# Optimization experiments

Hardware: AMD Instinct MI355X
Metric: run time of the kernel (lower is better)

The kernel has to match this reference:

```python
import jax, jax.numpy as jnp
import numpy as np

N_NODES = 50000
N_EDGES = 800000
N_GRAPHS = 64
IN_C = 256      # num_commodities
HID = 256       # hidden_units
HID2 = HID // 2
N_DCS = 64


def setup_inputs() -> dict:
    key = jax.random.key(0)
    ks = jax.random.split(key, 8)
    x = jax.random.normal(ks[0], (N_NODES, IN_C), dtype=jnp.float32)
    edge_index = jax.random.randint(ks[1], (2, N_EDGES), 0, N_NODES, dtype=jnp.int32)
    # sorted graph-membership ids; even partition guarantees no empty graph
    batch = ((jnp.arange(N_NODES) * N_GRAPHS) // N_NODES).astype(jnp.int32)
    s1 = 1.0 / np.sqrt(IN_C)
    s2 = 1.0 / np.sqrt(HID)
    s3 = 1.0 / np.sqrt(HID2)
    W1 = jax.random.normal(ks[2], (IN_C, HID), dtype=jnp.float32) * s1
    b1 = jnp.zeros((HID,), dtype=jnp.float32)
    W2 = jax.random.normal(ks[3], (HID, HID2), dtype=jnp.float32) * s2
    b2 = jnp.zeros((HID2,), dtype=jnp.float32)
    Wm = jax.random.normal(ks[4], (HID2, N_DCS), dtype=jnp.float32) * s3
    bm = jax.random.normal(ks[5], (N_DCS,), dtype=jnp.float32) * s3
    return {"x": x, "edge_index": edge_index, "batch": batch,
            "W1": W1, "b1": b1, "W2": W2, "b2": b2, "Wm": Wm, "bm": bm}


def gcn_conv(x, W, b, src, dst, n_nodes):
    """PyG GCNConv: D^{-1/2}(A+I)D^{-1/2} X W + b (self-loops added)."""
    h = x @ W                                    # [N, out]
    ones = jnp.ones(src.shape[0], dtype=h.dtype)
    deg = jax.ops.segment_sum(ones, dst, num_segments=n_nodes) + 1.0  # +1 self-loop
    dis = jax.lax.rsqrt(deg)                     # deg >= 1, safe
    norm = dis[src] * dis[dst]                   # [E]
    agg = jax.ops.segment_sum(h[src] * norm[:, None], dst, num_segments=n_nodes)
    agg = agg + h * (dis * dis)[:, None]         # self-loop contribution
    return agg + b


def reference(x, edge_index, batch, W1, b1, W2, b2, Wm, bm):
    src, dst = edge_index[0], edge_index[1]
    n = x.shape[0]
    bx = jax.nn.relu(gcn_conv(x, W1, b1, src, dst, n))
    cx = jax.nn.relu(gcn_conv(bx, W2, b2, src, dst, n))
    px = jax.ops.segment_max(cx, batch, num_segments=N_GRAPHS)  # global max pool
    return px @ Wm + bm                           # [N_GRAPHS, N_DCS]
```

## Files before the change

kernel.cpp:

```cpp
#include <hip/hip_runtime.h>
#include <cstdint>


typedef _Float16 half4v __attribute__((ext_vector_type(4)));
typedef _Float16 half8v __attribute__((ext_vector_type(8)));
typedef float f32x4 __attribute__((ext_vector_type(4)));

__device__ __forceinline__ void gl_lds16(const void* g, void* l) {
  __builtin_amdgcn_global_load_lds(
      (const __attribute__((address_space(1))) unsigned int*)g,
      (__attribute__((address_space(3))) unsigned int*)l, 16, 0, 0);
}

__global__ void count_deg_k(const int* __restrict__ dst, int* __restrict__ deg, int E) {
  int e = blockIdx.x * blockDim.x + threadIdx.x;
  if (e < E) atomicAdd(&deg[dst[e]], 1);
}

__global__ void dis_k(const int* __restrict__ deg, float* __restrict__ dis, int n) {
  int i = blockIdx.x * blockDim.x + threadIdx.x;
  if (i < n) dis[i] = 1.0f / sqrtf((float)deg[i] + 1.0f);
}

__global__ void scan1_k(const int* __restrict__ deg, int* __restrict__ blksum, int n) {
  __shared__ int sd[256];
  int i = blockIdx.x * 256 + threadIdx.x;
  sd[threadIdx.x] = (i < n) ? deg[i] : 0;
  __syncthreads();
  for (int s = 128; s > 0; s >>= 1) {
    if (threadIdx.x < s) sd[threadIdx.x] += sd[threadIdx.x + s];
    __syncthreads();
  }
  if (threadIdx.x == 0) blksum[blockIdx.x] = sd[0];
}

__global__ void scan2_k(const int* __restrict__ blksum, int* __restrict__ blkoff, int nb) {
  __shared__ int sd[256];
  int v = (threadIdx.x < nb) ? blksum[threadIdx.x] : 0;
  sd[threadIdx.x] = v;
  __syncthreads();
  for (int d = 1; d < 256; d <<= 1) {
    int t = (threadIdx.x >= d) ? sd[threadIdx.x - d] : 0;
    __syncthreads();
    sd[threadIdx.x] += t;
    __syncthreads();
  }
  if (threadIdx.x < nb) blkoff[threadIdx.x] = sd[threadIdx.x] - v;
}

__global__ void scan3_k(const int* __restrict__ deg, const int* __restrict__ blkoff,
                        int* __restrict__ offs, int n) {
  __shared__ int sd[256];
  int i = blockIdx.x * 256 + threadIdx.x;
  int v = (i < n) ? deg[i] : 0;
  sd[threadIdx.x] = v;
  __syncthreads();
  for (int d = 1; d < 256; d <<= 1) {
    int t = (threadIdx.x >= d) ? sd[threadIdx.x - d] : 0;
    __syncthreads();
    sd[threadIdx.x] += t;
    __syncthreads();
  }
  if (i < n) offs[i] = blkoff[blockIdx.x] + sd[threadIdx.x] - v;
  if (i == n - 1) offs[n] = blkoff[blockIdx.x] + sd[threadIdx.x];
}

__global__ void fill_csr_k(const int* __restrict__ src, const int* __restrict__ dst,
                           const int* __restrict__ offs, int* __restrict__ cursor,
                           int* __restrict__ csr, int E) {
  int e = blockIdx.x * blockDim.x + threadIdx.x;
  if (e >= E) return;
  int d = dst[e];
  int pos = atomicAdd(&cursor[d], 1);
  csr[offs[d] + pos] = src[e];
}

__global__ void cvt_x_k(const float* __restrict__ in, _Float16* __restrict__ out, int n4) {
  int i = blockIdx.x * blockDim.x + threadIdx.x;
  if (i < n4) {
    float4 v = ((const float4*)in)[i];
    half4v o = {(_Float16)v.x, (_Float16)v.y, (_Float16)v.z, (_Float16)v.w};
    ((half4v*)out)[i] = o;
  }
}

__global__ void cvtT_k(const float* __restrict__ W, _Float16* __restrict__ Wt, int K, int N) {
  int idx = blockIdx.x * 256 + threadIdx.x;
  if (idx < K * N) {
    int k = idx / N, c = idx - k * N;
    Wt[(size_t)c * K + k] = (_Float16)W[idx];
  }
}

#define GBM 128
#define GBN 128
#define GBK 32

__global__ __launch_bounds__(256) void gemm_f16(const _Float16* __restrict__ A,
                                                const _Float16* __restrict__ Bt,
                                                _Float16* __restrict__ C,
                                                int M, int N, int K) {
  __shared__ _Float16 As[GBM * GBK];
  __shared__ _Float16 Bs[GBN * GBK];
  const int tid = threadIdx.x;
  const int lane = tid & 63;
  const int wave = tid >> 6;
  const int wm = wave >> 1, wn = wave & 1;
  const int row0 = blockIdx.x * GBM;
  const int col0 = blockIdx.y * GBN;

  f32x4 acc[4][4] = {};

  const int kbase = (lane >> 4) * 8;
  const _Float16* aSrc[2];
  _Float16* aDst[2];
  const _Float16* bSrc[2];
  _Float16* bDst[2];
#pragma unroll
  for (int h = 0; h < 2; ++h) {
    int fl = h * 4 + wave;
    int row = h * 64 + wave * 16 + (lane & 15);
    int gr = row0 + row;
    if (gr > M - 1) gr = M - 1;
    aSrc[h] = A + (size_t)gr * K + kbase;
    aDst[h] = As + fl * 512;
    int gc = col0 + row;
    bSrc[h] = Bt + (size_t)gc * K + kbase;
    bDst[h] = Bs + fl * 512;
  }

  for (int k0 = 0; k0 < K; k0 += GBK) {
    gl_lds16(aSrc[0] + k0, aDst[0]);
    gl_lds16(aSrc[1] + k0, aDst[1]);
    gl_lds16(bSrc[0] + k0, bDst[0]);
    gl_lds16(bSrc[1] + k0, bDst[1]);
    __syncthreads();

    half8v af[4], bf[4];
#pragma unroll
    for (int m = 0; m < 4; ++m)
      af[m] = *(const half8v*)(As + (wm * 4 + m) * 512 + lane * 8);
#pragma unroll
    for (int nj = 0; nj < 4; ++nj)
      bf[nj] = *(const half8v*)(Bs + (wn * 4 + nj) * 512 + lane * 8);
#pragma unroll
    for (int m = 0; m < 4; ++m)
#pragma unroll
      for (int nj = 0; nj < 4; ++nj)
        acc[m][nj] = __builtin_amdgcn_mfma_f32_16x16x32_f16(af[m], bf[nj], acc[m][nj], 0, 0, 0);
    __syncthreads();
  }

#pragma unroll
  for (int m = 0; m < 4; ++m) {
#pragma unroll
    for (int nj = 0; nj < 4; ++nj) {
      int col = col0 + wn * 64 + nj * 16 + (lane & 15);
#pragma unroll
      for (int r = 0; r < 4; ++r) {
        int row = row0 + wm * 64 + m * 16 + (lane >> 4) * 4 + r;
        if (row < M) C[(size_t)row * N + col] = (_Float16)acc[m][nj][r];
      }
    }
  }
}

template <int C, bool POOL>
__global__ __launch_bounds__(256) void agg_k(const _Float16* __restrict__ h,
                                             const float* __restrict__ dis,
                                             const int* __restrict__ offs,
                                             const int* __restrict__ csr,
                                             const float* __restrict__ bias,
                                             const int* __restrict__ batch,
                                             void* __restrict__ outv, int n) {
  constexpr int LPR = C / 8;
  constexpr int EPW = 64 / LPR;
  const int tid = threadIdx.x;
  const int lane = tid & 63;
  const int wave = tid >> 6;
  const int slot = lane / LPR;
  const int ch0 = (lane % LPR) * 8;

  const int wid = blockIdx.x * 4 + wave;
  const bool valid = wid < n;
  const int node = valid ? wid : n - 1;

  const int beg = offs[node], end = offs[node + 1];
  float acc[8] = {};
  for (int jb = beg; jb < end; jb += EPW * 4) {
#pragma unroll
    for (int u = 0; u < 4; ++u) {
      int e = jb + u * EPW + slot;
      int ec = e < end ? e : end - 1;
      int s = csr[ec];
      float w = (e < end) ? dis[s] : 0.f;
      half8v hv = *(const half8v*)(h + (size_t)s * C + ch0);
#pragma unroll
      for (int v = 0; v < 8; ++v) acc[v] = fmaf((float)hv[v], w, acc[v]);
    }
  }

  if constexpr (EPW == 4) {
#pragma unroll
    for (int v = 0; v < 8; ++v) {
      acc[v] += __shfl_xor(acc[v], 16);
      acc[v] += __shfl_xor(acc[v], 32);
    }
  } else {
#pragma unroll
    for (int v = 0; v < 8; ++v) acc[v] += __shfl_xor(acc[v], 32);
  }

  const float di = dis[node];
  half8v sv = *(const half8v*)(h + (size_t)node * C + ch0);
  float4 blo = *(const float4*)(bias + ch0);
  float4 bhi = *(const float4*)(bias + ch0 + 4);
  const float bb[8] = {blo.x, blo.y, blo.z, blo.w, bhi.x, bhi.y, bhi.z, bhi.w};
  float res[8];
#pragma unroll
  for (int v = 0; v < 8; ++v)
    res[v] = fmaxf(acc[v] * di + (float)sv[v] * (di * di) + bb[v], 0.f);

  if constexpr (!POOL) {
    if (valid && lane < LPR) {
      half8v r;
#pragma unroll
      for (int v = 0; v < 8; ++v) r[v] = (_Float16)res[v];
      *(half8v*)((_Float16*)outv + (size_t)node * C + ch0) = r;
    }
  } else {
    __shared__ float pres[4][C];
    __shared__ int pg[4];
    __shared__ int uni;
    const int g = valid ? batch[node] : -1 - wave;
    if (lane < LPR) {
      *(f32x4*)&pres[wave][ch0] = f32x4{res[0], res[1], res[2], res[3]};
      *(f32x4*)&pres[wave][ch0 + 4] = f32x4{res[4], res[5], res[6], res[7]};
    }
    if (lane == 0) pg[wave] = g;
    __syncthreads();
    if (tid == 0) uni = (pg[0] == pg[1] && pg[1] == pg[2] && pg[2] == pg[3] && pg[0] >= 0);
    __syncthreads();
    float* px = (float*)outv;
    if (uni) {
      if (tid < C) {
        float m = fmaxf(fmaxf(pres[0][tid], pres[1][tid]),
                        fmaxf(pres[2][tid], pres[3][tid]));
        atomicMax((int*)&px[(size_t)pg[0] * C + tid], __float_as_int(m));
      }
    } else {
#pragma unroll
      for (int wv = 0; wv < 4; ++wv) {
        int gg = pg[wv];
        if (gg >= 0 && tid < C)
          atomicMax((int*)&px[(size_t)gg * C + tid], __float_as_int(pres[wv][tid]));
      }
    }
  }
}

__global__ void final_mm_k(const float* __restrict__ px, const float* __restrict__ Wm,
                           const float* __restrict__ bm, float* __restrict__ out) {
  int g = blockIdx.x;
  int c = threadIdx.x;
  float acc = bm[c];
#pragma unroll 8
  for (int k = 0; k < 128; ++k)
    acc = fmaf(px[g * 128 + k], Wm[k * 64 + c], acc);
  out[g * 64 + c] = acc;
}

extern "C" void kernel_launch(void* const* d_in, const int* in_sizes, int n_in,
                              void* d_out, int out_size, void* d_ws, size_t ws_size,
                              hipStream_t stream) {
  const float* x     = (const float*)d_in[0];
  const int*   ei    = (const int*)d_in[1];
  const int*   batch = (const int*)d_in[2];
  const float* W1    = (const float*)d_in[3];
  const float* b1    = (const float*)d_in[4];
  const float* W2    = (const float*)d_in[5];
  const float* b2    = (const float*)d_in[6];
  const float* Wm    = (const float*)d_in[7];
  const float* bm    = (const float*)d_in[8];
  float* out = (float*)d_out;

  const int E = in_sizes[1] / 2;
  const int n = in_sizes[2];
  const int IN_C = 256, HID = 256, HID2 = 128, NG = 64;
  const int* src = ei;
  const int* dst = ei + E;

  char* w = (char*)d_ws;
  size_t off = 0;
  auto alloc = [&](size_t bytes) -> void* {
    void* p = w + off;
    off = (off + bytes + 255) & ~(size_t)255;
    return p;
  };
  const int nb = (n + 255) / 256;
  int*      deg    = (int*)alloc((size_t)n * 4);
  int*      cursor = (int*)alloc((size_t)n * 4);
  float*    dis    = (float*)alloc((size_t)n * 4);
  int*      offs   = (int*)alloc((size_t)(n + 1) * 4);
  int*      blksum = (int*)alloc((size_t)nb * 4);
  int*      blkoff = (int*)alloc((size_t)nb * 4);
  int*      csr    = (int*)alloc((size_t)E * 4);
  float*    px     = (float*)alloc((size_t)NG * HID2 * 4);
  _Float16* xh     = (_Float16*)alloc((size_t)n * IN_C * 2);
  _Float16* Wt1    = (_Float16*)alloc((size_t)HID * IN_C * 2);
  _Float16* Wt2    = (_Float16*)alloc((size_t)HID2 * HID * 2);
  _Float16* bufA   = (_Float16*)alloc((size_t)n * HID * 2);
  _Float16* bufB   = (_Float16*)alloc((size_t)n * HID * 2);
  _Float16* h1 = bufA;
  _Float16* bx = bufB;
  _Float16* h2 = bufA;

  hipMemsetAsync(deg, 0, (size_t)n * 4, stream);
  hipMemsetAsync(cursor, 0, (size_t)n * 4, stream);
  hipMemsetAsync(px, 0, (size_t)NG * HID2 * 4, stream);

  count_deg_k<<<(E + 255) / 256, 256, 0, stream>>>(dst, deg, E);
  dis_k<<<(n + 255) / 256, 256, 0, stream>>>(deg, dis, n);
  scan1_k<<<nb, 256, 0, stream>>>(deg, blksum, n);
  scan2_k<<<1, 256, 0, stream>>>(blksum, blkoff, nb);
  scan3_k<<<nb, 256, 0, stream>>>(deg, blkoff, offs, n);
  fill_csr_k<<<(E + 255) / 256, 256, 0, stream>>>(src, dst, offs, cursor, csr, E);

  cvt_x_k<<<(n * IN_C / 4 + 255) / 256, 256, 0, stream>>>(x, xh, n * IN_C / 4);
  cvtT_k<<<(IN_C * HID + 255) / 256, 256, 0, stream>>>(W1, Wt1, IN_C, HID);
  cvtT_k<<<(HID * HID2 + 255) / 256, 256, 0, stream>>>(W2, Wt2, HID, HID2);

  dim3 g1((n + GBM - 1) / GBM, HID / GBN);
  gemm_f16<<<g1, 256, 0, stream>>>(xh, Wt1, h1, n, HID, IN_C);
  agg_k<256, false><<<(n + 3) / 4, 256, 0, stream>>>(h1, dis, offs, csr, b1, nullptr, bx, n);

  dim3 g2((n + GBM - 1) / GBM, HID2 / GBN);
  gemm_f16<<<g2, 256, 0, stream>>>(bx, Wt2, h2, n, HID2, HID);
  agg_k<128, true><<<(n + 3) / 4, 256, 0, stream>>>(h2, dis, offs, csr, b2, batch, px, n);

  final_mm_k<<<NG, 64, 0, stream>>>(px, Wm, bm, out);
}
```

Baseline: 355.2 us.

## Pre-scale GEMM output by degree norm and simplify aggregation with fp16 partial sums

Moves the source-side D^{-1/2} scaling into the GEMM epilogue, so aggregation becomes a plain sum with no per-edge dis gather. The self-loop term is folded into the same sum. The edge loop is split into a full-block path that accumulates in packed fp16 before widening, plus a remainder loop. Several small launches are merged: dis with scan1, the three conversion kernels into one, reuse of deg as the fill cursor via atomicSub, and one memset instead of three. fp16 partial sums and the pre-scaled fp16 h add some rounding error.

```diff
diff --git a/kernel.cpp b/kernel.cpp
--- a/kernel.cpp
+++ b/kernel.cpp
@@ -2,6 +2,7 @@
 #include <cstdint>
 
 
+typedef _Float16 half2v __attribute__((ext_vector_type(2)));
 typedef _Float16 half4v __attribute__((ext_vector_type(4)));
 typedef _Float16 half8v __attribute__((ext_vector_type(8)));
 typedef float f32x4 __attribute__((ext_vector_type(4)));
@@ -17,15 +18,13 @@
   if (e < E) atomicAdd(&deg[dst[e]], 1);
 }
 
-__global__ void dis_k(const int* __restrict__ deg, float* __restrict__ dis, int n) {
-  int i = blockIdx.x * blockDim.x + threadIdx.x;
-  if (i < n) dis[i] = 1.0f / sqrtf((float)deg[i] + 1.0f);
-}
-
-__global__ void scan1_k(const int* __restrict__ deg, int* __restrict__ blksum, int n) {
+__global__ void scan1_dis_k(const int* __restrict__ deg, int* __restrict__ blksum,
+                            float* __restrict__ dis, int n) {
   __shared__ int sd[256];
   int i = blockIdx.x * 256 + threadIdx.x;
-  sd[threadIdx.x] = (i < n) ? deg[i] : 0;
+  int d = (i < n) ? deg[i] : 0;
+  if (i < n) dis[i] = 1.0f / sqrtf((float)d + 1.0f);
+  sd[threadIdx.x] = d;
   __syncthreads();
   for (int s = 128; s > 0; s >>= 1) {
     if (threadIdx.x < s) sd[threadIdx.x] += sd[threadIdx.x + s];
@@ -66,29 +65,36 @@
 }
 
 __global__ void fill_csr_k(const int* __restrict__ src, const int* __restrict__ dst,
-                           const int* __restrict__ offs, int* __restrict__ cursor,
+                           const int* __restrict__ offs, int* __restrict__ deg,
                            int* __restrict__ csr, int E) {
   int e = blockIdx.x * blockDim.x + threadIdx.x;
   if (e >= E) return;
   int d = dst[e];
-  int pos = atomicAdd(&cursor[d], 1);
+  int pos = atomicSub(&deg[d], 1) - 1;
   csr[offs[d] + pos] = src[e];
 }
 
-__global__ void cvt_x_k(const float* __restrict__ in, _Float16* __restrict__ out, int n4) {
-  int i = blockIdx.x * blockDim.x + threadIdx.x;
-  if (i < n4) {
-    float4 v = ((const float4*)in)[i];
+__global__ void cvt_all_k(const float* __restrict__ x, _Float16* __restrict__ xh,
+                          const float* __restrict__ W1, _Float16* __restrict__ Wt1,
+                          const float* __restrict__ W2, _Float16* __restrict__ Wt2,
+                          int xn4) {
+  int i = blockIdx.x * 256 + threadIdx.x;
+  if (i < xn4) {
+    float4 v = ((const float4*)x)[i];
     half4v o = {(_Float16)v.x, (_Float16)v.y, (_Float16)v.z, (_Float16)v.w};
-    ((half4v*)out)[i] = o;
-  }
-}
-
-__global__ void cvtT_k(const float* __restrict__ W, _Float16* __restrict__ Wt, int K, int N) {
-  int idx = blockIdx.x * 256 + threadIdx.x;
-  if (idx < K * N) {
-    int k = idx / N, c = idx - k * N;
-    Wt[(size_t)c * K + k] = (_Float16)W[idx];
+    ((half4v*)xh)[i] = o;
+    return;
+  }
+  int j = i - xn4;
+  if (j < 256 * 256) {
+    int k = j >> 8, c = j & 255;
+    Wt1[c * 256 + k] = (_Float16)W1[j];
+    return;
+  }
+  j -= 256 * 256;
+  if (j < 256 * 128) {
+    int k = j >> 7, c = j & 127;
+    Wt2[c * 256 + k] = (_Float16)W2[j];
   }
 }
 
@@ -98,6 +104,7 @@
 
 __global__ __launch_bounds__(256) void gemm_f16(const _Float16* __restrict__ A,
                                                 const _Float16* __restrict__ Bt,
+                                                const float* __restrict__ dis,
                                                 _Float16* __restrict__ C,
                                                 int M, int N, int K) {
   __shared__ _Float16 As[GBM * GBK];
@@ -153,13 +160,17 @@
 
 #pragma unroll
   for (int m = 0; m < 4; ++m) {
+    const int rbase = row0 + wm * 64 + m * 16 + (lane >> 4) * 4;
+    float dr[4];
+#pragma unroll
+    for (int r = 0; r < 4; ++r) dr[r] = (rbase + r < M) ? dis[rbase + r] : 0.f;
 #pragma unroll
     for (int nj = 0; nj < 4; ++nj) {
       int col = col0 + wn * 64 + nj * 16 + (lane & 15);
 #pragma unroll
       for (int r = 0; r < 4; ++r) {
-        int row = row0 + wm * 64 + m * 16 + (lane >> 4) * 4 + r;
-        if (row < M) C[(size_t)row * N + col] = (_Float16)acc[m][nj][r];
+        int row = rbase + r;
+        if (row < M) C[(size_t)row * N + col] = (_Float16)(acc[m][nj][r] * dr[r]);
       }
     }
   }
@@ -175,6 +186,7 @@
                                              void* __restrict__ outv, int n) {
   constexpr int LPR = C / 8;
   constexpr int EPW = 64 / LPR;
+  constexpr int EBLK = EPW * 4;
   const int tid = threadIdx.x;
   const int lane = tid & 63;
   const int wave = tid >> 6;
@@ -187,17 +199,28 @@
 
   const int beg = offs[node], end = offs[node + 1];
   float acc[8] = {};
-  for (int jb = beg; jb < end; jb += EPW * 4) {
+  int jb = beg;
+  for (; jb + EBLK <= end; jb += EBLK) {
+    half2v ah[4] = {};
 #pragma unroll
     for (int u = 0; u < 4; ++u) {
-      int e = jb + u * EPW + slot;
-      int ec = e < end ? e : end - 1;
-      int s = csr[ec];
-      float w = (e < end) ? dis[s] : 0.f;
+      int s = csr[jb + u * EPW + slot];
       half8v hv = *(const half8v*)(h + (size_t)s * C + ch0);
-#pragma unroll
-      for (int v = 0; v < 8; ++v) acc[v] = fmaf((float)hv[v], w, acc[v]);
-    }
+      const half2v* hp = (const half2v*)&hv;
+#pragma unroll
+      for (int p = 0; p < 4; ++p) ah[p] += hp[p];
+    }
+#pragma unroll
+    for (int p = 0; p < 4; ++p) {
+      acc[2 * p + 0] += (float)ah[p][0];
+      acc[2 * p + 1] += (float)ah[p][1];
+    }
+  }
+  for (int e = jb + slot; e < end; e += EPW) {
+    int s = csr[e];
+    half8v hv = *(const half8v*)(h + (size_t)s * C + ch0);
+#pragma unroll
+    for (int v = 0; v < 8; ++v) acc[v] += (float)hv[v];
   }
 
   if constexpr (EPW == 4) {
@@ -219,7 +242,7 @@
   float res[8];
 #pragma unroll
   for (int v = 0; v < 8; ++v)
-    res[v] = fmaxf(acc[v] * di + (float)sv[v] * (di * di) + bb[v], 0.f);
+    res[v] = fmaxf((acc[v] + (float)sv[v]) * di + bb[v], 0.f);
 
   if constexpr (!POOL) {
     if (valid && lane < LPR) {
@@ -299,13 +322,13 @@
   };
   const int nb = (n + 255) / 256;
   int*      deg    = (int*)alloc((size_t)n * 4);
-  int*      cursor = (int*)alloc((size_t)n * 4);
+  float*    px     = (float*)alloc((size_t)NG * HID2 * 4);
+  size_t    zlen   = off;
   float*    dis    = (float*)alloc((size_t)n * 4);
   int*      offs   = (int*)alloc((size_t)(n + 1) * 4);
   int*      blksum = (int*)alloc((size_t)nb * 4);
   int*      blkoff = (int*)alloc((size_t)nb * 4);
   int*      csr    = (int*)alloc((size_t)E * 4);
-  float*    px     = (float*)alloc((size_t)NG * HID2 * 4);
   _Float16* xh     = (_Float16*)alloc((size_t)n * IN_C * 2);
   _Float16* Wt1    = (_Float16*)alloc((size_t)HID * IN_C * 2);
   _Float16* Wt2    = (_Float16*)alloc((size_t)HID2 * HID * 2);
@@ -315,27 +338,24 @@
   _Float16* bx = bufB;
   _Float16* h2 = bufA;
 
-  hipMemsetAsync(deg, 0, (size_t)n * 4, stream);
-  hipMemsetAsync(cursor, 0, (size_t)n * 4, stream);
-  hipMemsetAsync(px, 0, (size_t)NG * HID2 * 4, stream);
+  hipMemsetAsync(deg, 0, zlen, stream);
 
   count_deg_k<<<(E + 255) / 256, 256, 0, stream>>>(dst, deg, E);
-  dis_k<<<(n + 255) / 256, 256, 0, stream>>>(deg, dis, n);
-  scan1_k<<<nb, 256, 0, stream>>>(deg, blksum, n);
+  scan1_dis_k<<<nb, 256, 0, stream>>>(deg, blksum, dis, n);
   scan2_k<<<1, 256, 0, stream>>>(blksum, blkoff, nb);
   scan3_k<<<nb, 256, 0, stream>>>(deg, blkoff, offs, n);
-  fill_csr_k<<<(E + 255) / 256, 256, 0, stream>>>(src, dst, offs, cursor, csr, E);
-
-  cvt_x_k<<<(n * IN_C / 4 + 255) / 256, 256, 0, stream>>>(x, xh, n * IN_C / 4);
-  cvtT_k<<<(IN_C * HID + 255) / 256, 256, 0, stream>>>(W1, Wt1, IN_C, HID);
-  cvtT_k<<<(HID * HID2 + 255) / 256, 256, 0, stream>>>(W2, Wt2, HID, HID2);
+  fill_csr_k<<<(E + 255) / 256, 256, 0, stream>>>(src, dst, offs, deg, csr, E);
+
+  const int xn4 = n * IN_C / 4;
+  const int cvt_total = xn4 + 256 * 256 + 256 * 128;
+  cvt_all_k<<<(cvt_total + 255) / 256, 256, 0, stream>>>(x, xh, W1, Wt1, W2, Wt2, xn4);
 
   dim3 g1((n + GBM - 1) / GBM, HID / GBN);
-  gemm_f16<<<g1, 256, 0, stream>>>(xh, Wt1, h1, n, HID, IN_C);
+  gemm_f16<<<g1, 256, 0, stream>>>(xh, Wt1, dis, h1, n, HID, IN_C);
   agg_k<256, false><<<(n + 3) / 4, 256, 0, stream>>>(h1, dis, offs, csr, b1, nullptr, bx, n);
 
   dim3 g2((n + GBM - 1) / GBM, HID2 / GBN);
-  gemm_f16<<<g2, 256, 0, stream>>>(bx, Wt2, h2, n, HID2, HID);
+  gemm_f16<<<g2, 256, 0, stream>>>(bx, Wt2, dis, h2, n, HID2, HID);
   agg_k<128, true><<<(n + 3) / 4, 256, 0, stream>>>(h2, dis, offs, csr, b2, batch, px, n);
 
   final_mm_k<<<NG, 64, 0, stream>>>(px, Wm, bm, out);
```

Result: no change. 355.4 us (+0.1%).
